# Kernel optimization log

Hardware: AMD Instinct MI355X
Metric: run time of the kernel (lower is better)

Reference implementation:

```python
import jax, jax.numpy as jnp
import numpy as np

C_S, C_Z, MAX_LEN, N_AA, L = 256, 128, 1024, 21, 512
LN_EPS = 1e-5


def setup_inputs() -> dict:
    key = jax.random.key(0)
    ks = jax.random.split(key, 12)
    inp = {
        "seq": jax.random.randint(ks[0], (L,), 0, N_AA),
        "chain_id_res": jax.random.randint(ks[1], (L,), 0, 2),
        "res_idx": jax.random.randint(ks[2], (L,), 0, L),
        # learned parameters
        "E_aa": jax.random.normal(ks[3], (N_AA, C_S), jnp.float32) * 0.02,
        "E_pos": jax.random.normal(ks[4], (MAX_LEN, C_S), jnp.float32) * 0.02,
        "E_chain": jax.random.normal(ks[5], (2, C_S), jnp.float32) * 0.02,
        "E_chainpair": jax.random.normal(ks[6], (4, C_Z), jnp.float32) * 0.02,
        "E_relpos": jax.random.normal(ks[7], (66, C_Z), jnp.float32) * 0.02,
        "W_pair": jax.random.normal(ks[8], (3 * C_S, C_Z), jnp.float32) / np.sqrt(3 * C_S),
        "b_pair": jnp.zeros((C_Z,), jnp.float32),
        "ln_w": jnp.ones((C_S,), jnp.float32),
        "ln_b": jnp.zeros((C_S,), jnp.float32),
    }
    return inp


def reference(seq, chain_id_res, res_idx, E_aa, E_pos, E_chain, E_chainpair,
              E_relpos, W_pair, b_pair, ln_w, ln_b):
    # single rep: sum of three embedding lookups -> [L, c_s]
    s = E_aa[seq] + E_pos[res_idx] + E_chain[chain_id_res]

    # LayerNorm over last dim
    mu = jnp.mean(s, axis=-1, keepdims=True)
    var = jnp.mean(jnp.square(s - mu), axis=-1, keepdims=True)
    u = (s - mu) * jax.lax.rsqrt(var + LN_EPS) * ln_w + ln_b  # [L, c_s]

    # pair_proj(cat(u_i, u_j, u_i*u_j)) decomposed: W = [W1; W2; W3]
    W1, W2, W3 = W_pair[:C_S], W_pair[C_S:2 * C_S], W_pair[2 * C_S:]
    zi = u @ W1                                   # [L, c_z] per-i term
    zj = u @ W2                                   # [L, c_z] per-j term
    zx = jnp.einsum('ic,jc,cz->ijz', u, u, W3)    # cross term (u_i*u_j) @ W3
    z = zi[:, None, :] + zj[None, :, :] + zx + b_pair  # [L, L, c_z]

    # chain-pair and relative-position embeddings
    chain_pair = chain_id_res[:, None] * 2 + chain_id_res[None, :]  # [L, L] in [0,3]
    same_chain = chain_id_res[:, None] == chain_id_res[None, :]
    diff = res_idx[:, None] - res_idx[None, :]
    clipped = jnp.clip(diff, -32, 32) + 32
    relpos = jnp.where(same_chain, clipped, 65)  # cross-chain bucket = 65

    z = z + E_chainpair[chain_pair] + E_relpos[relpos]
    return s, z
```

## Files before the change

kernel.cpp:

```cpp
#include <hip/hip_runtime.h>
#include <hip/hip_bf16.h>

#define L 512
#define CS 256
#define CZ 128
#define LN_EPS 1e-5f

typedef _Float16 f16_t;
typedef f16_t f16x8 __attribute__((ext_vector_type(8)));
typedef float f32x4 __attribute__((ext_vector_type(4)));

__global__ __launch_bounds__(256) void k_prep(
    const int* __restrict__ seq, const int* __restrict__ cid,
    const int* __restrict__ ridx,
    const float* __restrict__ Eaa, const float* __restrict__ Epos,
    const float* __restrict__ Ech, const float* __restrict__ lnw,
    const float* __restrict__ lnb, const float* __restrict__ Wp,
    const float* __restrict__ bp, const float* __restrict__ Ecp,
    const float* __restrict__ Erp,
    float* __restrict__ s_out, f16_t* __restrict__ u2,
    float* __restrict__ zrow, float* __restrict__ zcol,
    f16_t* __restrict__ w3c, float* __restrict__ tab)
{
    __shared__ float su[CS];
    __shared__ float red[8];
    const int i = blockIdx.x;
    const int c = threadIdx.x;

    if (i < 128) {
        w3c[(c >> 3) * (CZ * 8) + i * 8 + (c & 7)] = (f16_t)Wp[(2 * CS + c) * CZ + i];
    } else if (i < 128 + 264) {
        const int b2 = i - 128;
        if (c < CZ)
            tab[b2 * CZ + c] = Ecp[(b2 / 66) * CZ + c] + Erp[(b2 % 66) * CZ + c];
    }

    const int sq = seq[i], ri = ridx[i], ci = cid[i];
    const float v = Eaa[sq * CS + c] + Epos[ri * CS + c] + Ech[ci * CS + c];
    s_out[i * CS + c] = v;

    float s1 = v, s2 = v * v;
    #pragma unroll
    for (int o = 32; o > 0; o >>= 1) {
        s1 += __shfl_down(s1, o, 64);
        s2 += __shfl_down(s2, o, 64);
    }
    const int wv = c >> 6, lane = c & 63;
    if (lane == 0) { red[wv * 2] = s1; red[wv * 2 + 1] = s2; }
    __syncthreads();
    const float S  = red[0] + red[2] + red[4] + red[6];
    const float SS = red[1] + red[3] + red[5] + red[7];
    const float mu  = S * (1.0f / CS);
    const float var = SS * (1.0f / CS) - mu * mu;
    const float rs  = rsqrtf(var + LN_EPS);
    const float u   = (v - mu) * rs * lnw[c] + lnb[c];
    u2[(c >> 3) * (L * 8) + i * 8 + (c & 7)] = (f16_t)u;
    su[c] = u;
    __syncthreads();

    const int z = c & 127;
    const int half = c >> 7;
    const float* W = Wp + half * CS * CZ + z;
    float a0 = 0, a1 = 0, a2 = 0, a3 = 0;
    #pragma unroll 8
    for (int cc = 0; cc < CS; cc += 4) {
        a0 += su[cc + 0] * W[(cc + 0) * CZ];
        a1 += su[cc + 1] * W[(cc + 1) * CZ];
        a2 += su[cc + 2] * W[(cc + 2) * CZ];
        a3 += su[cc + 3] * W[(cc + 3) * CZ];
    }
    const float acc = (a0 + a1) + (a2 + a3);
    if (half) zcol[i * CZ + z] = acc;
    else      zrow[i * CZ + z] = acc + bp[z];
}

__global__ __launch_bounds__(512, 2) void k_pair(
    const f16_t* __restrict__ u2, const f16_t* __restrict__ w3c,
    const float* __restrict__ zrow, const float* __restrict__ zcol,
    const float* __restrict__ tab,
    const int* __restrict__ cid, const int* __restrict__ ridx,
    float* __restrict__ zout)
{
    __shared__ f16_t lds[(1024 + 256) * 8];
    f16x8* lj = (f16x8*)lds;
    f16x8* li = ((f16x8*)lds) + 1024;

    const int t = threadIdx.x;
    const int lane = t & 63, wave = t >> 6;
    const int m = lane & 15, q = lane >> 4;
    const int j0 = blockIdx.x * 32, i0 = blockIdx.y * 8;
    const int jh = wave & 1;
    const int ih = (wave >> 1) & 1;
    const int zh = wave >> 2;
    const int jm = j0 + jh * 16 + m;
    const int ib = ih * 4;
    const int zb = zh * 64;

    const f16x8* pu = (const f16x8*)u2;
    const f16x8* pw = (const f16x8*)w3c;

    if (t < 256) li[t] = pu[(t >> 3) * L + i0 + (t & 7)];
    #pragma unroll
    for (int rep = 0; rep < 2; ++rep) {
        const int un = rep * 512 + t;
        lj[un] = pu[(un >> 5) * L + j0 + (un & 31)];
    }
    __syncthreads();

    f32x4 acc[4][4];
    #pragma unroll
    for (int ii = 0; ii < 4; ++ii)
        #pragma unroll
        for (int zt = 0; zt < 4; ++zt)
            acc[ii][zt] = (f32x4){0.f, 0.f, 0.f, 0.f};

    #pragma unroll
    for (int k32 = 0; k32 < 8; ++k32) {
        const int cb = k32 * 4 + q;
        f16x8 Az[4];
        #pragma unroll
        for (int zt = 0; zt < 4; ++zt)
            Az[zt] = pw[cb * CZ + zb + zt * 16 + m];
        const f16x8 ujv = lj[cb * 32 + jh * 16 + m];
        #pragma unroll
        for (int ii = 0; ii < 4; ++ii) {
            const f16x8 B = li[cb * 8 + ib + ii] * ujv;
            #pragma unroll
            for (int zt = 0; zt < 4; ++zt)
                acc[ii][zt] = __builtin_amdgcn_mfma_f32_16x16x32_f16(
                    Az[zt], B, acc[ii][zt], 0, 0, 0);
        }
    }

    const int cj = cid[jm], rj = ridx[jm];
    f32x4 ZC[4];
    #pragma unroll
    for (int zt = 0; zt < 4; ++zt)
        ZC[zt] = *(const f32x4*)&zcol[jm * CZ + zb + zt * 16 + q * 4];

    #pragma unroll
    for (int ii = 0; ii < 4; ++ii) {
        const int i = i0 + ib + ii;
        const int ci = cid[i], ri = ridx[i];
        int d = ri - rj; d = d < -32 ? -32 : (d > 32 ? 32 : d);
        const int x = ((ci * 2 + cj) * 66) + ((ci == cj) ? (d + 32) : 65);
        float* r_o = zout + ((size_t)i * L + jm) * CZ;
        #pragma unroll
        for (int zt = 0; zt < 4; ++zt) {
            const int zo = zb + zt * 16 + q * 4;
            const f32x4 zr = *(const f32x4*)&zrow[i * CZ + zo];
            const f32x4 tb = *(const f32x4*)&tab[x * CZ + zo];
            const f32x4 o = acc[ii][zt] + zr + ZC[zt] + tb;
            *(f32x4*)(r_o + zo) = o;
        }
    }
}

extern "C" void kernel_launch(void* const* d_in, const int* in_sizes, int n_in,
                              void* d_out, int out_size, void* d_ws, size_t ws_size,
                              hipStream_t stream) {
    const int*   seq  = (const int*)d_in[0];
    const int*   cid  = (const int*)d_in[1];
    const int*   ridx = (const int*)d_in[2];
    const float* Eaa  = (const float*)d_in[3];
    const float* Epos = (const float*)d_in[4];
    const float* Ech  = (const float*)d_in[5];
    const float* Ecp  = (const float*)d_in[6];
    const float* Erp  = (const float*)d_in[7];
    const float* Wp   = (const float*)d_in[8];
    const float* bp   = (const float*)d_in[9];
    const float* lnw  = (const float*)d_in[10];
    const float* lnb  = (const float*)d_in[11];

    float* out   = (float*)d_out;
    float* s_out = out;
    float* zout  = out + L * CS;

    char* ws = (char*)d_ws;
    f16_t* u2   = (f16_t*)ws;
    f16_t* w3c  = (f16_t*)(ws + 262144);
    float* zrow = (float*)(ws + 327680);
    float* zcol = (float*)(ws + 589824);
    float* tab  = (float*)(ws + 851968);

    hipLaunchKernelGGL(k_prep, dim3(L), dim3(256), 0, stream,
                       seq, cid, ridx, Eaa, Epos, Ech, lnw, lnb, Wp, bp,
                       Ecp, Erp, s_out, u2, zrow, zcol, w3c, tab);
    hipLaunchKernelGGL(k_pair, dim3(16, 64), dim3(512), 0, stream,
                       u2, w3c, zrow, zcol, tab, cid, ridx, zout);
}
```

Measured before the change: 193.8 us.

## Restructure pair kernel to stream i-pairs with register-resident W3 and prefetched epilogue

Each wave now holds its W3 fragments for a 32-wide z slice in registers across all 8 k-steps. It then loops over i in pairs, initialising the accumulators with the zrow+zcol+table bias and storing each pair as soon as it is done. The bias loads for the next i-pair are issued before the current stores, and the global loads are placed before the barrier so they overlap the LDS fill. Occupancy is raised to 4 blocks per CU, which lowers accumulator register pressure but constrains register allocation and serialises the i loop.

```diff
diff --git a/kernel.cpp b/kernel.cpp
--- a/kernel.cpp
+++ b/kernel.cpp
@@ -74,7 +74,7 @@
     else      zrow[i * CZ + z] = acc + bp[z];
 }
 
-__global__ __launch_bounds__(512, 2) void k_pair(
+__global__ __launch_bounds__(512, 4) void k_pair(
     const f16_t* __restrict__ u2, const f16_t* __restrict__ w3c,
     const float* __restrict__ zrow, const float* __restrict__ zcol,
     const float* __restrict__ tab,
@@ -89,12 +89,11 @@
     const int lane = t & 63, wave = t >> 6;
     const int m = lane & 15, q = lane >> 4;
     const int j0 = blockIdx.x * 32, i0 = blockIdx.y * 8;
-    const int jh = wave & 1;
-    const int ih = (wave >> 1) & 1;
-    const int zh = wave >> 2;
+    const int zsg = (wave & 3) * 32;
+    const int jh = wave >> 2;
     const int jm = j0 + jh * 16 + m;
-    const int ib = ih * 4;
-    const int zb = zh * 64;
+    const int zq0 = zsg + q * 4;
+    const int zq1 = zsg + 16 + q * 4;
 
     const f16x8* pu = (const f16x8*)u2;
     const f16x8* pw = (const f16x8*)w3c;
@@ -105,54 +104,61 @@
         const int un = rep * 512 + t;
         lj[un] = pu[(un >> 5) * L + j0 + (un & 31)];
     }
-    __syncthreads();
 
-    f32x4 acc[4][4];
-    #pragma unroll
-    for (int ii = 0; ii < 4; ++ii)
-        #pragma unroll
-        for (int zt = 0; zt < 4; ++zt)
-            acc[ii][zt] = (f32x4){0.f, 0.f, 0.f, 0.f};
-
+    f16x8 A0[8], A1[8];
     #pragma unroll
     for (int k32 = 0; k32 < 8; ++k32) {
-        const int cb = k32 * 4 + q;
-        f16x8 Az[4];
-        #pragma unroll
-        for (int zt = 0; zt < 4; ++zt)
-            Az[zt] = pw[cb * CZ + zb + zt * 16 + m];
-        const f16x8 ujv = lj[cb * 32 + jh * 16 + m];
-        #pragma unroll
-        for (int ii = 0; ii < 4; ++ii) {
-            const f16x8 B = li[cb * 8 + ib + ii] * ujv;
-            #pragma unroll
-            for (int zt = 0; zt < 4; ++zt)
-                acc[ii][zt] = __builtin_amdgcn_mfma_f32_16x16x32_f16(
-                    Az[zt], B, acc[ii][zt], 0, 0, 0);
-        }
+        A0[k32] = pw[(k32 * 4 + q) * CZ + zsg + m];
+        A1[k32] = pw[(k32 * 4 + q) * CZ + zsg + 16 + m];
     }
 
     const int cj = cid[jm], rj = ridx[jm];
-    f32x4 ZC[4];
-    #pragma unroll
-    for (int zt = 0; zt < 4; ++zt)
-        ZC[zt] = *(const f32x4*)&zcol[jm * CZ + zb + zt * 16 + q * 4];
+    const f32x4 ZC0 = *(const f32x4*)&zcol[jm * CZ + zq0];
+    const f32x4 ZC1 = *(const f32x4*)&zcol[jm * CZ + zq1];
 
-    #pragma unroll
-    for (int ii = 0; ii < 4; ++ii) {
-        const int i = i0 + ib + ii;
+    auto cinit = [&](int i, f32x4& c0, f32x4& c1) {
         const int ci = cid[i], ri = ridx[i];
         int d = ri - rj; d = d < -32 ? -32 : (d > 32 ? 32 : d);
         const int x = ((ci * 2 + cj) * 66) + ((ci == cj) ? (d + 32) : 65);
-        float* r_o = zout + ((size_t)i * L + jm) * CZ;
+        c0 = *(const f32x4*)&zrow[i * CZ + zq0] + ZC0
+           + *(const f32x4*)&tab[x * CZ + zq0];
+        c1 = *(const f32x4*)&zrow[i * CZ + zq1] + ZC1
+           + *(const f32x4*)&tab[x * CZ + zq1];
+    };
+
+    f32x4 c00, c01, c10, c11;
+    cinit(i0, c00, c01);
+    cinit(i0 + 1, c10, c11);
+
+    __syncthreads();
+
+    #pragma unroll 1
+    for (int ig = 0; ig < 4; ++ig) {
+        f32x4 a00 = c00, a01 = c01, a10 = c10, a11 = c11;
+
         #pragma unroll
-        for (int zt = 0; zt < 4; ++zt) {
-            const int zo = zb + zt * 16 + q * 4;
-            const f32x4 zr = *(const f32x4*)&zrow[i * CZ + zo];
-            const f32x4 tb = *(const f32x4*)&tab[x * CZ + zo];
-            const f32x4 o = acc[ii][zt] + zr + ZC[zt] + tb;
-            *(f32x4*)(r_o + zo) = o;
+        for (int k32 = 0; k32 < 8; ++k32) {
+            const int cb = k32 * 4 + q;
+            const f16x8 uj = lj[cb * 32 + jh * 16 + m];
+            const f16x8 B0 = li[cb * 8 + ig * 2] * uj;
+            const f16x8 B1 = li[cb * 8 + ig * 2 + 1] * uj;
+            a00 = __builtin_amdgcn_mfma_f32_16x16x32_f16(A0[k32], B0, a00, 0, 0, 0);
+            a01 = __builtin_amdgcn_mfma_f32_16x16x32_f16(A1[k32], B0, a01, 0, 0, 0);
+            a10 = __builtin_amdgcn_mfma_f32_16x16x32_f16(A0[k32], B1, a10, 0, 0, 0);
+            a11 = __builtin_amdgcn_mfma_f32_16x16x32_f16(A1[k32], B1, a11, 0, 0, 0);
         }
+
+        if (ig < 3) {
+            cinit(i0 + ig * 2 + 2, c00, c01);
+            cinit(i0 + ig * 2 + 3, c10, c11);
+        }
+
+        float* r0 = zout + ((size_t)(i0 + ig * 2) * L + jm) * CZ;
+        float* r1 = r0 + (size_t)L * CZ;
+        *(f32x4*)(r0 + zq0) = a00;
+        *(f32x4*)(r0 + zq1) = a01;
+        *(f32x4*)(r1 + zq0) = a10;
+        *(f32x4*)(r1 + zq1) = a11;
     }
 }
 
```

Measured after the change: 224.4 us. 1.16x slower.

## Remap pair waves to 2 rows by full z, preload bias into accumulators

Applied to the files above, without the earlier changes.

Each wave now handles two i rows and all 128 z channels instead of four rows and half the channels. The B operands (u_i*u_j) are built once and pinned in registers, and the W3 A-fragments are double-buffered across z-tile pairs in a non-unrolled loop. The row, column and table bias terms are loaded into the accumulators before the MFMAs, so the epilogue is only stores and that load latency can overlap the LDS sync. This raises register pressure and turns the z loop into a serial loop, which may hurt occupancy or instruction scheduling in a store-bound kernel.

```diff
diff --git a/kernel.cpp b/kernel.cpp
--- a/kernel.cpp
+++ b/kernel.cpp
@@ -9,6 +9,8 @@
 typedef _Float16 f16_t;
 typedef f16_t f16x8 __attribute__((ext_vector_type(8)));
 typedef float f32x4 __attribute__((ext_vector_type(4)));
+
+#define PIN4(x) asm volatile("" : "+v"(reinterpret_cast<f32x4&>(x)))
 
 __global__ __launch_bounds__(256) void k_prep(
     const int* __restrict__ seq, const int* __restrict__ cid,
@@ -90,11 +92,9 @@
     const int m = lane & 15, q = lane >> 4;
     const int j0 = blockIdx.x * 32, i0 = blockIdx.y * 8;
     const int jh = wave & 1;
-    const int ih = (wave >> 1) & 1;
-    const int zh = wave >> 2;
+    const int iw = wave >> 1;
     const int jm = j0 + jh * 16 + m;
-    const int ib = ih * 4;
-    const int zb = zh * 64;
+    const int ia = i0 + iw * 2, ib = ia + 1;
 
     const f16x8* pu = (const f16x8*)u2;
     const f16x8* pw = (const f16x8*)w3c;
@@ -105,54 +105,75 @@
         const int un = rep * 512 + t;
         lj[un] = pu[(un >> 5) * L + j0 + (un & 31)];
     }
+
+    const int cj = cid[jm], rj = ridx[jm];
+    const int cia = cid[ia], ria = ridx[ia];
+    const int cib = cid[ib], rib = ridx[ib];
+    int d;
+    d = ria - rj; d = d < -32 ? -32 : (d > 32 ? 32 : d);
+    const int xa = ((cia * 2 + cj) * 66) + ((cia == cj) ? (d + 32) : 65);
+    d = rib - rj; d = d < -32 ? -32 : (d > 32 ? 32 : d);
+    const int xb = ((cib * 2 + cj) * 66) + ((cib == cj) ? (d + 32) : 65);
+
+    f32x4 acc[2][8];
+    #pragma unroll
+    for (int zt = 0; zt < 8; ++zt) {
+        const int zq = zt * 16 + q * 4;
+        const f32x4 ZC = *(const f32x4*)&zcol[jm * CZ + zq];
+        acc[0][zt] = *(const f32x4*)&zrow[ia * CZ + zq] + ZC
+                   + *(const f32x4*)&tab[xa * CZ + zq];
+        acc[1][zt] = *(const f32x4*)&zrow[ib * CZ + zq] + ZC
+                   + *(const f32x4*)&tab[xb * CZ + zq];
+    }
+
     __syncthreads();
 
-    f32x4 acc[4][4];
-    #pragma unroll
-    for (int ii = 0; ii < 4; ++ii)
-        #pragma unroll
-        for (int zt = 0; zt < 4; ++zt)
-            acc[ii][zt] = (f32x4){0.f, 0.f, 0.f, 0.f};
-
-    #pragma unroll
-    for (int k32 = 0; k32 < 8; ++k32) {
-        const int cb = k32 * 4 + q;
-        f16x8 Az[4];
-        #pragma unroll
-        for (int zt = 0; zt < 4; ++zt)
-            Az[zt] = pw[cb * CZ + zb + zt * 16 + m];
-        const f16x8 ujv = lj[cb * 32 + jh * 16 + m];
-        #pragma unroll
-        for (int ii = 0; ii < 4; ++ii) {
-            const f16x8 B = li[cb * 8 + ib + ii] * ujv;
+    f16x8 B0[8], B1[8];
+    #pragma unroll
+    for (int k = 0; k < 8; ++k) {
+        const int cb = k * 4 + q;
+        const f16x8 uj  = lj[cb * 32 + jh * 16 + m];
+        B0[k] = li[cb * 8 + iw * 2]     * uj;
+        B1[k] = li[cb * 8 + iw * 2 + 1] * uj;
+    }
+    #pragma unroll
+    for (int k = 0; k < 8; ++k) { PIN4(B0[k]); PIN4(B1[k]); }
+
+    f16x8 A_a[8], A_b[8];
+    #pragma unroll
+    for (int k = 0; k < 8; ++k)
+        A_a[k] = pw[(k * 4 + q) * CZ + 0 * 16 + m];
+
+    #pragma unroll 1
+    for (int zp = 0; zp < 4; ++zp) {
+        const int zt0 = zp * 2, zt1 = zt0 + 1;
+        #pragma unroll
+        for (int k = 0; k < 8; ++k)
+            A_b[k] = pw[(k * 4 + q) * CZ + zt1 * 16 + m];
+        #pragma unroll
+        for (int k = 0; k < 8; ++k) {
+            acc[0][zt0] = __builtin_amdgcn_mfma_f32_16x16x32_f16(A_a[k], B0[k], acc[0][zt0], 0, 0, 0);
+            acc[1][zt0] = __builtin_amdgcn_mfma_f32_16x16x32_f16(A_a[k], B1[k], acc[1][zt0], 0, 0, 0);
+        }
+        if (zp < 3) {
             #pragma unroll
-            for (int zt = 0; zt < 4; ++zt)
-                acc[ii][zt] = __builtin_amdgcn_mfma_f32_16x16x32_f16(
-                    Az[zt], B, acc[ii][zt], 0, 0, 0);
+            for (int k = 0; k < 8; ++k)
+                A_a[k] = pw[(k * 4 + q) * CZ + (zt0 + 2) * 16 + m];
         }
-    }
-
-    const int cj = cid[jm], rj = ridx[jm];
-    f32x4 ZC[4];
-    #pragma unroll
-    for (int zt = 0; zt < 4; ++zt)
-        ZC[zt] = *(const f32x4*)&zcol[jm * CZ + zb + zt * 16 + q * 4];
-
-    #pragma unroll
-    for (int ii = 0; ii < 4; ++ii) {
-        const int i = i0 + ib + ii;
-        const int ci = cid[i], ri = ridx[i];
-        int d = ri - rj; d = d < -32 ? -32 : (d > 32 ? 32 : d);
-        const int x = ((ci * 2 + cj) * 66) + ((ci == cj) ? (d + 32) : 65);
-        float* r_o = zout + ((size_t)i * L + jm) * CZ;
-        #pragma unroll
-        for (int zt = 0; zt < 4; ++zt) {
-            const int zo = zb + zt * 16 + q * 4;
-            const f32x4 zr = *(const f32x4*)&zrow[i * CZ + zo];
-            const f32x4 tb = *(const f32x4*)&tab[x * CZ + zo];
-            const f32x4 o = acc[ii][zt] + zr + ZC[zt] + tb;
-            *(f32x4*)(r_o + zo) = o;
+        #pragma unroll
+        for (int k = 0; k < 8; ++k) {
+            acc[0][zt1] = __builtin_amdgcn_mfma_f32_16x16x32_f16(A_b[k], B0[k], acc[0][zt1], 0, 0, 0);
+            acc[1][zt1] = __builtin_amdgcn_mfma_f32_16x16x32_f16(A_b[k], B1[k], acc[1][zt1], 0, 0, 0);
         }
+    }
+
+    {
+        float* ra = zout + ((size_t)ia * L + jm) * CZ + q * 4;
+        float* rb = zout + ((size_t)ib * L + jm) * CZ + q * 4;
+        #pragma unroll
+        for (int zt = 0; zt < 8; ++zt) *(f32x4*)(ra + zt * 16) = acc[0][zt];
+        #pragma unroll
+        for (int zt = 0; zt < 8; ++zt) *(f32x4*)(rb + zt * 16) = acc[1][zt];
     }
 }
 
```

Measured after the change: 255.3 us. 31.7% more time.
